# Kernel optimization log

Measured on AMD Instinct MI355X. Metric: run time of the kernel, lower is better.

Reference implementation:

```python
import jax, jax.numpy as jnp
import numpy as np

N_NODES = 50000
N_EDGES = 800000
D_IN, D_HID, D_OUT = 64, 128, 64


def _sage_conv(x, src, dst, W_l, b_l, W_r):
    # PyG SAGEConv (aggr='mean'): out = lin_l(mean_j x_j) + lin_r(x_i)
    msg = x[src]                                    # [E, d] gather
    summed = jax.ops.segment_sum(msg, dst, num_segments=N_NODES)
    cnt = jax.ops.segment_sum(jnp.ones((msg.shape[0], 1), x.dtype), dst,
                              num_segments=N_NODES)
    mean = summed / jnp.maximum(cnt, 1.0)           # [N, d]
    return mean @ W_l + b_l + x @ W_r


def setup_inputs() -> dict:
    key = jax.random.key(0)
    ks = jax.random.split(key, 8)
    x = jax.random.normal(ks[0], (N_NODES, D_IN), dtype=jnp.float32)
    edge_index = jax.random.randint(ks[1], (2, N_EDGES), 0, N_NODES, dtype=jnp.int64)
    s1 = 1.0 / np.sqrt(D_IN)
    s2 = 1.0 / np.sqrt(D_HID)
    W_l1 = jax.random.uniform(ks[2], (D_IN, D_HID), jnp.float32, -s1, s1)
    b_l1 = jnp.zeros((D_HID,), jnp.float32)
    W_r1 = jax.random.uniform(ks[3], (D_IN, D_HID), jnp.float32, -s1, s1)
    W_l2 = jax.random.uniform(ks[4], (D_HID, D_OUT), jnp.float32, -s2, s2)
    b_l2 = jnp.zeros((D_OUT,), jnp.float32)
    W_r2 = jax.random.uniform(ks[5], (D_HID, D_OUT), jnp.float32, -s2, s2)
    return {"x": x, "edge_index": edge_index,
            "W_l1": W_l1, "b_l1": b_l1, "W_r1": W_r1,
            "W_l2": W_l2, "b_l2": b_l2, "W_r2": W_r2}


def reference(x, edge_index, W_l1, b_l1, W_r1, W_l2, b_l2, W_r2):
    src, dst = edge_index[0], edge_index[1]
    h = _sage_conv(x, src, dst, W_l1, b_l1, W_r1)
    h = jax.nn.relu(h)
    # dropout is identity in eval mode (F.dropout(training=self.training))
    out = _sage_conv(h, src, dst, W_l2, b_l2, W_r2)
    return out
```

## Files before the change

### kernel.cpp

```cpp
#include <hip/hip_runtime.h>

namespace {

constexpr int NNODES = 50000;
constexpr int NEDGES = 800000;
constexpr int NBUCK  = (NNODES + 127) / 128;
constexpr int BCAP   = 3072;
constexpr int SB     = 64;
constexpr int CHUNK  = NEDGES / SB;


static __device__ __forceinline__ unsigned short f2bf(float f) {
  unsigned u = __float_as_uint(f);
  u += 0x7FFFu + ((u >> 16) & 1u);
  return (unsigned short)(u >> 16);
}
static __device__ __forceinline__ float bf2f(unsigned short b) {
  return __uint_as_float((unsigned)b << 16);
}

static __device__ __forceinline__ int detect_is64_block(const void* raw, int* s_tmp) {
  if (threadIdx.x == 0) *s_tmp = 0;
  __syncthreads();
  const unsigned int* w = (const unsigned int*)raw;
  const int nz = (w[1 + 2 * (int)threadIdx.x] != 0u) ? 1 : 0;
  if (nz) atomicOr(s_tmp, 1);
  __syncthreads();
  return (*s_tmp == 0) ? 1 : 0;
}

__global__ __launch_bounds__(256) void x_to_bf16(const float* __restrict__ xin,
                                                 unsigned short* __restrict__ xb) {
  const int total4 = NNODES * 64 / 4;
  const int stride = gridDim.x * blockDim.x;
  for (int t = blockIdx.x * blockDim.x + threadIdx.x; t < total4; t += stride) {
    const float4 v = ((const float4*)xin)[t];
    ushort4 o;
    o.x = f2bf(v.x); o.y = f2bf(v.y); o.z = f2bf(v.z); o.w = f2bf(v.w);
    ((ushort4*)xb)[t] = o;
  }
}

__global__ __launch_bounds__(512) void hist_pass(const void* __restrict__ raw,
                                                 int* __restrict__ blkhist) {
  __shared__ int hist[NBUCK];
  __shared__ int s_tmp;
  const int is64 = detect_is64_block(raw, &s_tmp);
  for (int i = threadIdx.x; i < NBUCK; i += 512) hist[i] = 0;
  __syncthreads();
  const int b = blockIdx.x;
  const int beg = b * CHUNK, end = beg + CHUNK;
  for (int e = beg + (int)threadIdx.x; e < end; e += 512) {
    const int d = is64 ? (int)((const long long*)raw)[NEDGES + e]
                       : ((const int*)raw)[NEDGES + e];
    atomicAdd(&hist[d >> 7], 1);
  }
  __syncthreads();
  for (int i = threadIdx.x; i < NBUCK; i += 512) blkhist[i * SB + b] = hist[i];
}

__global__ __launch_bounds__(64) void col_scan(const int* __restrict__ blkhist,
                                               int* __restrict__ offs,
                                               int* __restrict__ bcount) {
  const int bk = blockIdx.x;
  const int t = threadIdx.x;
  const int c = blkhist[bk * SB + t];
  int s = c;
#pragma unroll
  for (int off = 1; off < 64; off <<= 1) {
    const int u = __shfl_up(s, off, 64);
    if (t >= off) s += u;
  }
  offs[bk * SB + t] = bk * BCAP + (s - c);
  if (t == 63) bcount[bk] = s;
}

__global__ __launch_bounds__(512) void bucket_prefix(const int* __restrict__ bcount,
                                                     int* __restrict__ bprefix) {
  __shared__ int sh[512];
  const int t = threadIdx.x;
  const int v = (t < NBUCK) ? bcount[t] : 0;
  sh[t] = v;
  __syncthreads();
#pragma unroll
  for (int off = 1; off < 512; off <<= 1) {
    const int val = sh[t];
    const int add = (t >= off) ? sh[t - off] : 0;
    __syncthreads();
    sh[t] = val + add;
    __syncthreads();
  }
  if (t < NBUCK) bprefix[t] = sh[t] - v;
}

__global__ __launch_bounds__(512) void scatter_pass(const void* __restrict__ raw,
                                                    const int* __restrict__ offs,
                                                    unsigned int* __restrict__ ebuf) {
  __shared__ int loff[NBUCK];
  __shared__ int lcur[NBUCK];
  __shared__ int s_tmp;
  const int is64 = detect_is64_block(raw, &s_tmp);
  const int b = blockIdx.x;
  for (int i = threadIdx.x; i < NBUCK; i += 512) {
    loff[i] = offs[i * SB + b];
    lcur[i] = 0;
  }
  __syncthreads();
  const int beg = b * CHUNK, end = beg + CHUNK;
  for (int e = beg + (int)threadIdx.x; e < end; e += 512) {
    int s, d;
    if (is64) {
      const long long* p = (const long long*)raw;
      s = (int)p[e];
      d = (int)p[NEDGES + e];
    } else {
      const int* p = (const int*)raw;
      s = p[e];
      d = p[NEDGES + e];
    }
    const int bk = d >> 7;
    const unsigned int val = ((unsigned int)d << 16) | (unsigned int)s;
    const int lr = atomicAdd(&lcur[bk], 1);
    ebuf[loff[bk] + lr] = val;
  }
}

__global__ __launch_bounds__(256) void csr_emit2(const unsigned int* __restrict__ ebuf,
                                                 const int* __restrict__ bcount,
                                                 const int* __restrict__ bprefix,
                                                 int* __restrict__ row_ptr,
                                                 int* __restrict__ col) {
  const int bk = blockIdx.x;
  const int base = bk * 128;
  const int nloc = min(128, NNODES - base);
  const int cnt = bcount[bk];
  const int bbase = bprefix[bk];
  const unsigned int* eb = ebuf + (size_t)bk * BCAP;

  __shared__ int dcnt[128];
  __shared__ int loff[128];
  __shared__ int lcur[128];
  if (threadIdx.x < 128) dcnt[threadIdx.x] = 0;
  __syncthreads();

  unsigned int vals[12];
  int m = 0;
#pragma unroll
  for (int k = 0; k < 12; ++k) {
    const int e = (int)threadIdx.x + k * 256;
    if (e < cnt) {
      vals[k] = eb[e];
      atomicAdd(&dcnt[(vals[k] >> 16) & 127u], 1);
      m = k + 1;
    }
  }
  __syncthreads();

  if (threadIdx.x < 128) loff[threadIdx.x] = dcnt[threadIdx.x];
  __syncthreads();
#pragma unroll
  for (int off = 1; off < 128; off <<= 1) {
    int add = 0;
    if (threadIdx.x < 128 && (int)threadIdx.x >= off) add = loff[threadIdx.x - off];
    __syncthreads();
    if (threadIdx.x < 128) loff[threadIdx.x] += add;
    __syncthreads();
  }
  if (threadIdx.x < 128) {
    const int excl = loff[threadIdx.x] - dcnt[threadIdx.x];
    loff[threadIdx.x] = excl;
    lcur[threadIdx.x] = 0;
    if ((int)threadIdx.x < nloc) row_ptr[base + threadIdx.x] = bbase + excl;
  }
  if (bk == NBUCK - 1 && threadIdx.x == 0) row_ptr[NNODES] = NEDGES;
  __syncthreads();

#pragma unroll
  for (int k = 0; k < 12; ++k) {
    if (k < m) {
      const int loc = (int)((vals[k] >> 16) & 127u);
      const int slot = bbase + loff[loc] + atomicAdd(&lcur[loc], 1);
      col[slot] = (int)(vals[k] & 0xFFFFu);
    }
  }
}

template <bool FINAL>
__global__ __launch_bounds__(256) void seg_mean_bf(const unsigned short* __restrict__ xb,
                                                   const int* __restrict__ row_ptr,
                                                   const int* __restrict__ col,
                                                   const float* __restrict__ radd,
                                                   float* __restrict__ outbuf) {
  const int lane = threadIdx.x & 63;
  const int wid = (blockIdx.x * blockDim.x + threadIdx.x) >> 6;
  const int nw = (gridDim.x * blockDim.x) >> 6;
  for (int v = wid; v < NNODES; v += nw) {
    const int b = row_ptr[v];
    const int e = row_ptr[v + 1];
    float acc = 0.0f;
    int i = b;
    for (; i + 4 <= e; i += 4) {
      const int s0 = col[i], s1 = col[i + 1], s2 = col[i + 2], s3 = col[i + 3];
      const float v0 = bf2f(xb[(size_t)s0 * 64 + lane]);
      const float v1 = bf2f(xb[(size_t)s1 * 64 + lane]);
      const float v2 = bf2f(xb[(size_t)s2 * 64 + lane]);
      const float v3 = bf2f(xb[(size_t)s3 * 64 + lane]);
      acc += (v0 + v1) + (v2 + v3);
    }
    for (; i < e; ++i) acc += bf2f(xb[(size_t)col[i] * 64 + lane]);
    const float inv = 1.0f / fmaxf((float)(e - b), 1.0f);
    float val = acc * inv;
    if (FINAL) val += radd[(size_t)v * 64 + lane];
    outbuf[(size_t)v * 64 + lane] = val;
  }
}

template <int MODE>
__global__ __launch_bounds__(256, 3) void gemm128(const float* __restrict__ A0,
                                                  const float* __restrict__ A1,
                                                  const float* __restrict__ W0,
                                                  const float* __restrict__ W1,
                                                  const float* __restrict__ bias,
                                                  float* __restrict__ O0,
                                                  float* __restrict__ O1,
                                                  unsigned short* __restrict__ PB) {
  constexpr int SAS = 36;
  __shared__ float sA[64][SAS];
  __shared__ float sW[32][128];
  const int row0 = blockIdx.x * 64;
  const int tid = threadIdx.x;
  const int rowgrp = tid >> 4;
  const int colgrp = tid & 15;
  const int r0 = rowgrp * 4;
  const int j0 = colgrp * 4;

  float accA[4][4];
  float accB[4][4];
#pragma unroll
  for (int r = 0; r < 4; ++r)
#pragma unroll
    for (int c = 0; c < 4; ++c) { accA[r][c] = 0.0f; accB[r][c] = 0.0f; }

#pragma unroll 1
  for (int ck = 0; ck < 4; ++ck) {
#pragma unroll
    for (int v = 0; v < 2; ++v) {
      const int vid = v * 256 + tid;
      const int rr = vid >> 3;
      const int kq = (vid & 7) * 4;
      const int grow = row0 + rr;
      float4 val = make_float4(0.f, 0.f, 0.f, 0.f);
      if (grow < NNODES) {
        if (MODE == 0) {
          const float* src = (ck < 2) ? A0 : A1;
          const int kk = (ck & 1) * 32 + kq;
          val = *(const float4*)&src[(size_t)grow * 64 + kk];
        } else {
          val = *(const float4*)&A0[(size_t)grow * 128 + ck * 32 + kq];
        }
      }
      *(float4*)&sA[rr][kq] = val;
    }
#pragma unroll
    for (int v = 0; v < 4; ++v) {
      const int vid = v * 256 + tid;
      const int kk = vid >> 5;
      const int jq = (vid & 31) * 4;
      float4 w;
      if (MODE == 0) {
        const float* src = (ck < 2) ? W0 : W1;
        const int krel = (ck & 1) * 32 + kk;
        w = *(const float4*)&src[(size_t)krel * 128 + jq];
      } else {
        const int kg = ck * 32 + kk;
        const float* src = (jq < 64) ? W0 : W1;
        const int jrel = (jq < 64) ? jq : jq - 64;
        w = *(const float4*)&src[(size_t)kg * 64 + jrel];
      }
      *(float4*)&sW[kk][jq] = w;
    }
    __syncthreads();
#pragma unroll
    for (int k4 = 0; k4 < 8; ++k4) {
      float4 a[4];
#pragma unroll
      for (int r = 0; r < 4; ++r) a[r] = *(const float4*)&sA[r0 + r][k4 * 4];
#pragma unroll
      for (int ki = 0; ki < 4; ++ki) {
        const float4 wlo = *(const float4*)&sW[k4 * 4 + ki][j0];
        const float4 whi = *(const float4*)&sW[k4 * 4 + ki][64 + j0];
#pragma unroll
        for (int r = 0; r < 4; ++r) {
          const float av = (ki == 0) ? a[r].x : (ki == 1) ? a[r].y
                         : (ki == 2) ? a[r].z : a[r].w;
          accA[r][0] = fmaf(av, wlo.x, accA[r][0]);
          accA[r][1] = fmaf(av, wlo.y, accA[r][1]);
          accA[r][2] = fmaf(av, wlo.z, accA[r][2]);
          accA[r][3] = fmaf(av, wlo.w, accA[r][3]);
          accB[r][0] = fmaf(av, whi.x, accB[r][0]);
          accB[r][1] = fmaf(av, whi.y, accB[r][1]);
          accB[r][2] = fmaf(av, whi.z, accB[r][2]);
          accB[r][3] = fmaf(av, whi.w, accB[r][3]);
        }
      }
    }
    __syncthreads();
  }

  float4 blo = make_float4(0.f, 0.f, 0.f, 0.f);
  float4 bhi;
  if (MODE == 0) {
    blo = *(const float4*)&bias[j0];
    bhi = *(const float4*)&bias[64 + j0];
  } else {
    bhi = *(const float4*)&bias[j0];
  }
#pragma unroll
  for (int r = 0; r < 4; ++r) {
    const int grow = row0 + r0 + r;
    if (grow >= NNODES) continue;
    float4 lo = make_float4(accA[r][0] + blo.x, accA[r][1] + blo.y,
                            accA[r][2] + blo.z, accA[r][3] + blo.w);
    float4 hi = make_float4(accB[r][0] + bhi.x, accB[r][1] + bhi.y,
                            accB[r][2] + bhi.z, accB[r][3] + bhi.w);
    if (MODE == 0) {
      lo.x = fmaxf(lo.x, 0.f); lo.y = fmaxf(lo.y, 0.f);
      lo.z = fmaxf(lo.z, 0.f); lo.w = fmaxf(lo.w, 0.f);
      hi.x = fmaxf(hi.x, 0.f); hi.y = fmaxf(hi.y, 0.f);
      hi.z = fmaxf(hi.z, 0.f); hi.w = fmaxf(hi.w, 0.f);
      *(float4*)&O0[(size_t)grow * 128 + j0] = lo;
      *(float4*)&O0[(size_t)grow * 128 + 64 + j0] = hi;
    } else {
      ushort4 ob;
      ob.x = f2bf(lo.x); ob.y = f2bf(lo.y); ob.z = f2bf(lo.z); ob.w = f2bf(lo.w);
      *(ushort4*)&PB[(size_t)grow * 64 + j0] = ob;
      *(float4*)&O1[(size_t)grow * 64 + j0] = hi;
    }
  }
}

}

extern "C" void kernel_launch(void* const* d_in, const int* in_sizes, int n_in,
                              void* d_out, int out_size, void* d_ws, size_t ws_size,
                              hipStream_t stream) {
  const float* x   = (const float*)d_in[0];
  const void*  ei  = d_in[1];
  const float* Wl1 = (const float*)d_in[2];
  const float* bl1 = (const float*)d_in[3];
  const float* Wr1 = (const float*)d_in[4];
  const float* Wl2 = (const float*)d_in[5];
  const float* bl2 = (const float*)d_in[6];
  const float* Wr2 = (const float*)d_in[7];
  float* out = (float*)d_out;

  char* ws = (char*)d_ws;
  int*            blkhist = (int*)(ws + 0);
  int*            offs    = (int*)(ws + 100352);
  int*            bcount  = (int*)(ws + 200704);
  int*            bprefix = (int*)(ws + 202752);
  int*            row_ptr = (int*)(ws + 204800);
  int*            col     = (int*)(ws + 404992);
  unsigned int*   ebuf    = (unsigned int*)(ws + 3604992);
  unsigned short* xb      = (unsigned short*)(ws + 8409600);
  unsigned short* pb      = (unsigned short*)(ws + 14809600);
  float*          mean1   = (float*)(ws + 21209600);
  float*          h       = (float*)(ws + 34009600);
  float*          r       = mean1;

  x_to_bf16<<<1024, 256, 0, stream>>>(x, xb);

  hist_pass<<<SB, 512, 0, stream>>>(ei, blkhist);
  col_scan<<<NBUCK, 64, 0, stream>>>(blkhist, offs, bcount);
  bucket_prefix<<<1, 512, 0, stream>>>(bcount, bprefix);
  scatter_pass<<<SB, 512, 0, stream>>>(ei, offs, ebuf);
  csr_emit2<<<NBUCK, 256, 0, stream>>>(ebuf, bcount, bprefix, row_ptr, col);

  constexpr int GEMM_BLOCKS = (NNODES + 63) / 64;

  seg_mean_bf<false><<<12500, 256, 0, stream>>>(xb, row_ptr, col, nullptr, mean1);
  gemm128<0><<<GEMM_BLOCKS, 256, 0, stream>>>(mean1, x, Wl1, Wr1, bl1, h, nullptr, nullptr);

  gemm128<1><<<GEMM_BLOCKS, 256, 0, stream>>>(h, nullptr, Wl2, Wr2, bl2, nullptr, r, pb);
  seg_mean_bf<true><<<12500, 256, 0, stream>>>(pb, row_ptr, col, r, out);
}
```

Baseline: 172.4 us.

## Gather two edges per wave with packed bf16 loads and use packed FMA in GEMM

The segment-mean kernel now has each half-wave read a 32-bit word holding two bf16 features, so one wave covers two neighbour rows per load. The halves are combined with a cross-half shuffle, and outputs are written as float2. Separately, the GEMM inner loop uses v_pk_fma_f32 inline assembly to do two FMAs per instruction. The aim is to cut gather instruction count and raise FMA throughput, at the cost of an extra shuffle, idle upper lanes during the store, and inline asm that may constrain register allocation.

```diff
diff --git a/kernel.cpp b/kernel.cpp
--- a/kernel.cpp
+++ b/kernel.cpp
@@ -15,8 +15,14 @@
   u += 0x7FFFu + ((u >> 16) & 1u);
   return (unsigned short)(u >> 16);
 }
-static __device__ __forceinline__ float bf2f(unsigned short b) {
-  return __uint_as_float((unsigned)b << 16);
+
+static __device__ __forceinline__ void pk_fma_lo(float2& d, const float2 a, const float2 b) {
+  asm("v_pk_fma_f32 %0, %1, %2, %0 op_sel:[0,0,0] op_sel_hi:[0,1,1]"
+      : "+v"(d) : "v"(a), "v"(b));
+}
+static __device__ __forceinline__ void pk_fma_hi(float2& d, const float2 a, const float2 b) {
+  asm("v_pk_fma_f32 %0, %1, %2, %0 op_sel:[1,0,0] op_sel_hi:[1,1,1]"
+      : "+v"(d) : "v"(a), "v"(b));
 }
 
 static __device__ __forceinline__ int detect_is64_block(const void* raw, int* s_tmp) {
@@ -186,32 +192,57 @@
 }
 
 template <bool FINAL>
-__global__ __launch_bounds__(256) void seg_mean_bf(const unsigned short* __restrict__ xb,
+__global__ __launch_bounds__(256) void seg_mean_bf(const unsigned int* __restrict__ xb2,
                                                    const int* __restrict__ row_ptr,
                                                    const int* __restrict__ col,
                                                    const float* __restrict__ radd,
                                                    float* __restrict__ outbuf) {
-  const int lane = threadIdx.x & 63;
+  const int lane = (int)(threadIdx.x & 63);
+  const int half = lane >> 5;
+  const int c = lane & 31;
   const int wid = (blockIdx.x * blockDim.x + threadIdx.x) >> 6;
   const int nw = (gridDim.x * blockDim.x) >> 6;
   for (int v = wid; v < NNODES; v += nw) {
     const int b = row_ptr[v];
     const int e = row_ptr[v + 1];
-    float acc = 0.0f;
+    float accx = 0.0f, accy = 0.0f;
     int i = b;
-    for (; i + 4 <= e; i += 4) {
-      const int s0 = col[i], s1 = col[i + 1], s2 = col[i + 2], s3 = col[i + 3];
-      const float v0 = bf2f(xb[(size_t)s0 * 64 + lane]);
-      const float v1 = bf2f(xb[(size_t)s1 * 64 + lane]);
-      const float v2 = bf2f(xb[(size_t)s2 * 64 + lane]);
-      const float v3 = bf2f(xb[(size_t)s3 * 64 + lane]);
-      acc += (v0 + v1) + (v2 + v3);
-    }
-    for (; i < e; ++i) acc += bf2f(xb[(size_t)col[i] * 64 + lane]);
-    const float inv = 1.0f / fmaxf((float)(e - b), 1.0f);
-    float val = acc * inv;
-    if (FINAL) val += radd[(size_t)v * 64 + lane];
-    outbuf[(size_t)v * 64 + lane] = val;
+    for (; i + 8 <= e; i += 8) {
+      const int s0 = col[i + 0 + half];
+      const int s1 = col[i + 2 + half];
+      const int s2 = col[i + 4 + half];
+      const int s3 = col[i + 6 + half];
+      const unsigned int w0 = xb2[(size_t)s0 * 32 + c];
+      const unsigned int w1 = xb2[(size_t)s1 * 32 + c];
+      const unsigned int w2 = xb2[(size_t)s2 * 32 + c];
+      const unsigned int w3 = xb2[(size_t)s3 * 32 + c];
+      accx += __uint_as_float(w0 << 16) + __uint_as_float(w1 << 16)
+            + __uint_as_float(w2 << 16) + __uint_as_float(w3 << 16);
+      accy += __uint_as_float(w0 & 0xFFFF0000u) + __uint_as_float(w1 & 0xFFFF0000u)
+            + __uint_as_float(w2 & 0xFFFF0000u) + __uint_as_float(w3 & 0xFFFF0000u);
+    }
+    for (; i + 2 <= e; i += 2) {
+      const unsigned int w0 = xb2[(size_t)col[i + half] * 32 + c];
+      accx += __uint_as_float(w0 << 16);
+      accy += __uint_as_float(w0 & 0xFFFF0000u);
+    }
+    if (i < e && half == 0) {
+      const unsigned int w0 = xb2[(size_t)col[i] * 32 + c];
+      accx += __uint_as_float(w0 << 16);
+      accy += __uint_as_float(w0 & 0xFFFF0000u);
+    }
+    accx += __shfl_xor(accx, 32, 64);
+    accy += __shfl_xor(accy, 32, 64);
+    if (half == 0) {
+      const float inv = 1.0f / fmaxf((float)(e - b), 1.0f);
+      float2 res = make_float2(accx * inv, accy * inv);
+      const size_t gi = (size_t)v * 32 + c;
+      if (FINAL) {
+        const float2 ra = ((const float2*)radd)[gi];
+        res.x += ra.x; res.y += ra.y;
+      }
+      ((float2*)outbuf)[gi] = res;
+    }
   }
 }
 
@@ -229,17 +260,18 @@
   __shared__ float sW[32][128];
   const int row0 = blockIdx.x * 64;
   const int tid = threadIdx.x;
-  const int rowgrp = tid >> 4;
-  const int colgrp = tid & 15;
-  const int r0 = rowgrp * 4;
-  const int j0 = colgrp * 4;
-
-  float accA[4][4];
-  float accB[4][4];
+  const int r0 = (tid >> 4) * 4;
+  const int j0 = (tid & 15) * 4;
+
+  float2 accA2[4][2];
+  float2 accB2[4][2];
 #pragma unroll
   for (int r = 0; r < 4; ++r)
 #pragma unroll
-    for (int c = 0; c < 4; ++c) { accA[r][c] = 0.0f; accB[r][c] = 0.0f; }
+    for (int p = 0; p < 2; ++p) {
+      accA2[r][p] = make_float2(0.f, 0.f);
+      accB2[r][p] = make_float2(0.f, 0.f);
+    }
 
 #pragma unroll 1
   for (int ck = 0; ck < 4; ++ck) {
@@ -286,21 +318,24 @@
 #pragma unroll
       for (int r = 0; r < 4; ++r) a[r] = *(const float4*)&sA[r0 + r][k4 * 4];
 #pragma unroll
-      for (int ki = 0; ki < 4; ++ki) {
-        const float4 wlo = *(const float4*)&sW[k4 * 4 + ki][j0];
-        const float4 whi = *(const float4*)&sW[k4 * 4 + ki][64 + j0];
+      for (int kp = 0; kp < 2; ++kp) {
+        const int k_even = k4 * 4 + kp * 2;
+        const float4 wlo0 = *(const float4*)&sW[k_even][j0];
+        const float4 whi0 = *(const float4*)&sW[k_even][64 + j0];
+        const float4 wlo1 = *(const float4*)&sW[k_even + 1][j0];
+        const float4 whi1 = *(const float4*)&sW[k_even + 1][64 + j0];
 #pragma unroll
         for (int r = 0; r < 4; ++r) {
-          const float av = (ki == 0) ? a[r].x : (ki == 1) ? a[r].y
-                         : (ki == 2) ? a[r].z : a[r].w;
-          accA[r][0] = fmaf(av, wlo.x, accA[r][0]);
-          accA[r][1] = fmaf(av, wlo.y, accA[r][1]);
-          accA[r][2] = fmaf(av, wlo.z, accA[r][2]);
-          accA[r][3] = fmaf(av, wlo.w, accA[r][3]);
-          accB[r][0] = fmaf(av, whi.x, accB[r][0]);
-          accB[r][1] = fmaf(av, whi.y, accB[r][1]);
-          accB[r][2] = fmaf(av, whi.z, accB[r][2]);
-          accB[r][3] = fmaf(av, whi.w, accB[r][3]);
+          const float2 ap = (kp == 0) ? make_float2(a[r].x, a[r].y)
+                                      : make_float2(a[r].z, a[r].w);
+          pk_fma_lo(accA2[r][0], ap, make_float2(wlo0.x, wlo0.y));
+          pk_fma_lo(accA2[r][1], ap, make_float2(wlo0.z, wlo0.w));
+          pk_fma_lo(accB2[r][0], ap, make_float2(whi0.x, whi0.y));
+          pk_fma_lo(accB2[r][1], ap, make_float2(whi0.z, whi0.w));
+          pk_fma_hi(accA2[r][0], ap, make_float2(wlo1.x, wlo1.y));
+          pk_fma_hi(accA2[r][1], ap, make_float2(wlo1.z, wlo1.w));
+          pk_fma_hi(accB2[r][0], ap, make_float2(whi1.x, whi1.y));
+          pk_fma_hi(accB2[r][1], ap, make_float2(whi1.z, whi1.w));
         }
       }
     }
@@ -319,10 +354,10 @@
   for (int r = 0; r < 4; ++r) {
     const int grow = row0 + r0 + r;
     if (grow >= NNODES) continue;
-    float4 lo = make_float4(accA[r][0] + blo.x, accA[r][1] + blo.y,
-                            accA[r][2] + blo.z, accA[r][3] + blo.w);
-    float4 hi = make_float4(accB[r][0] + bhi.x, accB[r][1] + bhi.y,
-                            accB[r][2] + bhi.z, accB[r][3] + bhi.w);
+    float4 lo = make_float4(accA2[r][0].x + blo.x, accA2[r][0].y + blo.y,
+                            accA2[r][1].x + blo.z, accA2[r][1].y + blo.w);
+    float4 hi = make_float4(accB2[r][0].x + bhi.x, accB2[r][0].y + bhi.y,
+                            accB2[r][1].x + bhi.z, accB2[r][1].y + bhi.w);
     if (MODE == 0) {
       lo.x = fmaxf(lo.x, 0.f); lo.y = fmaxf(lo.y, 0.f);
       lo.z = fmaxf(lo.z, 0.f); lo.w = fmaxf(lo.w, 0.f);
@@ -378,9 +413,11 @@
 
   constexpr int GEMM_BLOCKS = (NNODES + 63) / 64;
 
-  seg_mean_bf<false><<<12500, 256, 0, stream>>>(xb, row_ptr, col, nullptr, mean1);
+  seg_mean_bf<false><<<12500, 256, 0, stream>>>((const unsigned int*)xb, row_ptr, col,
+                                                nullptr, mean1);
   gemm128<0><<<GEMM_BLOCKS, 256, 0, stream>>>(mean1, x, Wl1, Wr1, bl1, h, nullptr, nullptr);
 
   gemm128<1><<<GEMM_BLOCKS, 256, 0, stream>>>(h, nullptr, Wl2, Wr2, bl2, nullptr, r, pb);
-  seg_mean_bf<true><<<12500, 256, 0, stream>>>(pb, row_ptr, col, r, out);
-}
+  seg_mean_bf<true><<<12500, 256, 0, stream>>>((const unsigned int*)pb, row_ptr, col,
+                                               r, out);
+}
```

Measured after the change: 163.6 us. 1.05x faster.
